# Optimization experiments

Measured on AMD Instinct MI355X. Metric: run time of the kernel, lower is better.

Reference implementation:

```python
import jax, jax.numpy as jnp
import numpy as np

N = 50000  # nodes (spots)


def setup_inputs() -> dict:
    key = jax.random.key(0)
    ks = jax.random.split(key, 10)
    d_gene, d_img, H, Hh, O = 3000, 1024, 512, 256, 64

    def lin(k, i, o):
        return (jax.random.normal(k, (i, o), jnp.float32) / np.sqrt(i).astype(np.float32))

    return {
        "gene_data": jax.random.normal(ks[0], (N, d_gene), jnp.float32),
        "image_data": jax.random.normal(ks[1], (N, d_img), jnp.float32),
        "gene_edge_index": jax.random.randint(ks[2], (2, 800000), 0, N, dtype=jnp.int32).astype(jnp.int64),
        "spatial_edge_index": jax.random.randint(ks[3], (2, 300000), 0, N, dtype=jnp.int32).astype(jnp.int64),
        "W_fc1": lin(ks[4], d_gene, H), "b_fc1": jnp.zeros((H,), jnp.float32),
        "W_fc2": lin(ks[5], d_img, H), "b_fc2": jnp.zeros((H,), jnp.float32),
        "W_g11": lin(ks[6], H, Hh), "b_g11": jnp.zeros((Hh,), jnp.float32),
        "W_g12": lin(ks[7], H, Hh), "b_g12": jnp.zeros((Hh,), jnp.float32),
        "W_g21": lin(ks[8], Hh, O), "b_g21": jnp.zeros((O,), jnp.float32),
        "W_g22": lin(ks[9], Hh, O), "b_g22": jnp.zeros((O,), jnp.float32),
        "w1": jnp.float32(0.5), "w2": jnp.float32(0.5),
    }


def _gcn(x, edge_index, W, b, n):
    # PyG GCNConv: h = x @ W; add self-loops; symmetric norm D^-1/2 (A+I) D^-1/2; scatter-add; + bias
    h = x @ W  # [n, out]
    loop = jnp.arange(n, dtype=edge_index.dtype)
    src = jnp.concatenate([edge_index[0], loop])
    dst = jnp.concatenate([edge_index[1], loop])
    deg = jax.ops.segment_sum(jnp.ones_like(src, x.dtype), dst, num_segments=n)
    dinv = jax.lax.rsqrt(jnp.maximum(deg, jnp.asarray(1e-12, x.dtype)))
    norm = dinv[src] * dinv[dst]  # [E+n]
    out = jax.ops.segment_sum(h[src] * norm[:, None], dst, num_segments=n)
    return out + b


def reference(gene_data, image_data, gene_edge_index, spatial_edge_index,
              W_fc1, b_fc1, W_fc2, b_fc2,
              W_g11, b_g11, W_g12, b_g12,
              W_g21, b_g21, W_g22, b_g22,
              w1, w2):
    n = gene_data.shape[0]
    x1 = jax.nn.relu(gene_data @ W_fc1 + b_fc1)
    x2 = jax.nn.relu(image_data @ W_fc2 + b_fc2)
    # dropout: eval mode -> identity
    h1 = jax.nn.relu(_gcn(x1, spatial_edge_index, W_g11, b_g11, n))
    h2 = jax.nn.relu(_gcn(x2, gene_edge_index, W_g12, b_g12, n))
    x = w1 * h1 + (1.0 - w1) * h2
    o1 = _gcn(x, spatial_edge_index, W_g21, b_g21, n)
    o2 = _gcn(x, gene_edge_index, W_g22, b_g22, n)
    return w2 * o1 + (1.0 - w2) * o2
```

## Files before the change

### kernel.cpp

```cpp
#include <hip/hip_runtime.h>
#include <hip/hip_bf16.h>
#include <stdint.h>

typedef __attribute__((ext_vector_type(4))) float f32x4;
typedef __attribute__((ext_vector_type(8))) short short8;
typedef __attribute__((ext_vector_type(4))) short short4v;

#define CDIV(a, b) (((a) + (b) - 1) / (b))

__device__ __forceinline__ unsigned short f2bf(float x) {
  union { float f; unsigned int u; } c; c.f = x;
  unsigned int r = c.u + 0x7FFFu + ((c.u >> 16) & 1u);
  return (unsigned short)(r >> 16);
}
__device__ __forceinline__ unsigned short f2bf_hw(float x) {
  __hip_bfloat16 h = __float2bfloat16(x);
  unsigned short u; __builtin_memcpy(&u, &h, 2); return u;
}
__device__ __forceinline__ float bf2f(unsigned short b) {
  union { unsigned int u; float f; } c; c.u = (unsigned int)b << 16; return c.f;
}

__device__ __forceinline__ void gl2lds16(const void* g, void* lds) {
  __builtin_amdgcn_global_load_lds(
      reinterpret_cast<const __attribute__((address_space(1))) unsigned int*>(
          reinterpret_cast<uintptr_t>(g)),
      reinterpret_cast<__attribute__((address_space(3))) unsigned int*>(
          reinterpret_cast<uintptr_t>(lds)),
      16, 0, 0);
}

__global__ void transpose_w(const float* __restrict__ W, unsigned short* __restrict__ Wt,
                            int K, int N, int Kpad) {
  __shared__ float tile[32][33];
  int kb = blockIdx.x * 32, nb = blockIdx.y * 32;
  int tx = threadIdx.x & 31, ty = threadIdx.x >> 5;
  for (int r = ty; r < 32; r += 8) {
    int k = kb + r, n = nb + tx;
    tile[r][tx] = (k < K && n < N) ? W[(size_t)k * N + n] : 0.f;
  }
  __syncthreads();
  for (int r = ty; r < 32; r += 8) {
    int n = nb + r, k = kb + tx;
    if (n < N && k < Kpad) Wt[(size_t)n * Kpad + k] = f2bf(tile[tx][r]);
  }
}

__global__ void prep_init(int* __restrict__ dA, int* __restrict__ dB,
                          int* __restrict__ cA, int* __restrict__ cB, int n) {
  int i = blockIdx.x * blockDim.x + threadIdx.x;
  if (i < n) { dA[i] = 1; dB[i] = 1; cA[i] = 0; cB[i] = 0; }
}

__global__ void deg_hist_both(const int* __restrict__ eiA, int EA, int* __restrict__ degA,
                              const int* __restrict__ eiB, int EB, int* __restrict__ degB, int n) {
  int e = blockIdx.x * blockDim.x + threadIdx.x;
  if (e < EA) {
    unsigned int d = (unsigned int)eiA[(size_t)EA + e];
    if (d < (unsigned int)n) atomicAdd(&degA[d], 1);
  } else if (e < EA + EB) {
    int e2 = e - EA;
    unsigned int d = (unsigned int)eiB[(size_t)EB + e2];
    if (d < (unsigned int)n) atomicAdd(&degB[d], 1);
  }
}

__global__ void dinv_both(const int* __restrict__ dA, float* __restrict__ vA,
                          const int* __restrict__ dB, float* __restrict__ vB, int n) {
  int i = blockIdx.x * blockDim.x + threadIdx.x;
  if (i < n) { vA[i] = rsqrtf((float)dA[i]); vB[i] = rsqrtf((float)dB[i]); }
}

__global__ void scan_rowptr_dual(const int* __restrict__ degA, int* __restrict__ rpA,
                                 const int* __restrict__ degB, int* __restrict__ rpB, int n) {
  const int* deg = (blockIdx.x == 0) ? degA : degB;
  int* rp = (blockIdx.x == 0) ? rpA : rpB;
  __shared__ int wsum[16];
  __shared__ int carry_s;
  const int tid = threadIdx.x, lane = tid & 63, w = tid >> 6;
  if (tid == 0) carry_s = 0;
  __syncthreads();
  for (int base = 0; base < n; base += 1024) {
    int i = base + tid;
    int d = (i < n) ? (deg[i] - 1) : 0;
    int v = d;
    #pragma unroll
    for (int off = 1; off < 64; off <<= 1) {
      int t = __shfl_up(v, off, 64);
      if (lane >= off) v += t;
    }
    if (lane == 63) wsum[w] = v;
    __syncthreads();
    int carry = carry_s;
    if (w == 0) {
      int s = (lane < 16) ? wsum[lane] : 0;
      #pragma unroll
      for (int off = 1; off < 16; off <<= 1) {
        int t = __shfl_up(s, off, 64);
        if (lane >= off) s += t;
      }
      if (lane < 16) wsum[lane] = s;
    }
    __syncthreads();
    int woff = (w > 0) ? wsum[w - 1] : 0;
    if (i < n) rp[i] = carry + woff + v - d;
    if (tid == 0) carry_s = carry + wsum[15];
    __syncthreads();
  }
  if (threadIdx.x == 0) rp[n] = carry_s;
}

__global__ void csr_fill_both(const int* __restrict__ eiA, int EA, const int* __restrict__ rpA,
                              int* __restrict__ curA, const float* __restrict__ dvA,
                              int* __restrict__ csA, float* __restrict__ cnA,
                              const int* __restrict__ eiB, int EB, const int* __restrict__ rpB,
                              int* __restrict__ curB, const float* __restrict__ dvB,
                              int* __restrict__ csB, float* __restrict__ cnB, int n) {
  int e = blockIdx.x * blockDim.x + threadIdx.x;
  if (e < EA) {
    unsigned int s = (unsigned int)eiA[e];
    unsigned int d = (unsigned int)eiA[(size_t)EA + e];
    if (s < (unsigned int)n && d < (unsigned int)n) {
      int pos = rpA[d] + atomicAdd(&curA[d], 1);
      csA[pos] = (int)s;
      cnA[pos] = dvA[s] * dvA[d];
    }
  } else if (e < EA + EB) {
    int e2 = e - EA;
    unsigned int s = (unsigned int)eiB[e2];
    unsigned int d = (unsigned int)eiB[(size_t)EB + e2];
    if (s < (unsigned int)n && d < (unsigned int)n) {
      int pos = rpB[d] + atomicAdd(&curB[d], 1);
      csB[pos] = (int)s;
      cnB[pos] = dvB[s] * dvB[d];
    }
  }
}

template<int BM, int BN, int TH, int NT_N, int AMODE, bool ADD_BIAS, bool DO_RELU>
__global__ __launch_bounds__(TH, 2)
void gemm7(const void* __restrict__ Av, const unsigned short* __restrict__ Bt,
           const float* __restrict__ bias, unsigned short* __restrict__ C,
           int NT_M, int M, int N, int K, int Kpad) {
  constexpr int BK = 64;
  constexpr int WN = TH / 64;
  constexpr int WCOLS = BN / WN;
  constexpr int FM = BM / 16, FN = WCOLS / 16;
  constexpr int BIT  = (BN * 8) / TH;
  constexpr int AIT1 = (BM * 8) / TH;
  constexpr int AIT3 = (BM * 16) / TH;
  constexpr int LOGN = (NT_N == 4) ? 2 : (NT_N == 2 ? 1 : 0);

  const int bid = blockIdx.x;
  const int xcd = bid & 7, j = bid >> 3;
  const int per = (NT_M + 7) >> 3;
  const int mt = xcd * per + (j >> LOGN);
  const int nt = j & (NT_N - 1);
  if (mt >= NT_M) return;
  const int gm = mt * BM, gn = nt * BN;

  constexpr int ABYTES = (AMODE == 3) ? BM * BK * 4 : BM * BK * 2;
  __shared__ __align__(16) char AldsRaw[ABYTES];
  __shared__ __align__(16) unsigned short Blds[BN * BK];

  const int tid = threadIdx.x;
  const int wid = tid >> 6, lane = tid & 63;
  const int kg = lane >> 4, lr = lane & 15;
  const int sx = lr & 7;

  f32x4 acc[FM][FN] = {};

  const int nkt = Kpad / BK;
  for (int kt = 0; kt < nkt; ++kt) {
    const int k0 = kt * BK;
    if constexpr (AMODE == 1) {
      const unsigned short* A = (const unsigned short*)Av;
      unsigned short* Alds = (unsigned short*)AldsRaw;
      #pragma unroll
      for (int it = 0; it < AIT1; ++it) {
        int q = it * TH + tid;
        int r = q >> 3, s = q & 7;
        int grow = gm + r; if (grow > M - 1) grow = M - 1;
        gl2lds16(A + (size_t)grow * K + k0 + ((s ^ (r & 7)) << 3), &Alds[q * 8]);
      }
    } else {
      const float* A = (const float*)Av;
      float* Af = (float*)AldsRaw;
      if (k0 + BK <= K) {
        #pragma unroll
        for (int it = 0; it < AIT3; ++it) {
          int q = it * TH + tid;
          int r = q >> 4, s = q & 15;
          int grow = gm + r; if (grow > M - 1) grow = M - 1;
          gl2lds16(A + (size_t)grow * K + k0 + ((s ^ (r & 15)) << 2), &Af[q * 4]);
        }
      } else {
        #pragma unroll
        for (int it = 0; it < AIT3; ++it) {
          int q = it * TH + tid;
          int r = q >> 4, s = q & 15;
          int grow = gm + r; if (grow > M - 1) grow = M - 1;
          int kbase = k0 + ((s ^ (r & 15)) << 2);
          f32x4 v = {0.f, 0.f, 0.f, 0.f};
          if (kbase + 4 <= K) v = *(const f32x4*)(A + (size_t)grow * K + kbase);
          *(f32x4*)(&Af[q * 4]) = v;
        }
      }
    }
    #pragma unroll
    for (int it = 0; it < BIT; ++it) {
      int q = it * TH + tid;
      int r = q >> 3, s = q & 7;
      gl2lds16(Bt + (size_t)(gn + r) * Kpad + k0 + ((s ^ (r & 7)) << 3), &Blds[q * 8]);
    }
    __syncthreads();
    #pragma unroll
    for (int ks = 0; ks < 2; ++ks) {
      const int k8 = ks * 4 + kg;
      short8 af[FM];
      #pragma unroll
      for (int m = 0; m < FM; m++) {
        int r = m * 16 + lr;
        if constexpr (AMODE == 1) {
          const unsigned short* Alds = (const unsigned short*)AldsRaw;
          af[m] = *(const short8*)(&Alds[(r * 8 + (k8 ^ sx)) * 8]);
        } else {
          const float* Af = (const float*)AldsRaw;
          int s0 = (2 * k8) ^ lr, s1 = (2 * k8 + 1) ^ lr;
          f32x4 lo = *(const f32x4*)(Af + r * 64 + s0 * 4);
          f32x4 hi = *(const f32x4*)(Af + r * 64 + s1 * 4);
          #pragma unroll
          for (int i = 0; i < 4; i++) {
            af[m][i]     = (short)f2bf_hw(lo[i]);
            af[m][i + 4] = (short)f2bf_hw(hi[i]);
          }
        }
      }
      #pragma unroll
      for (int n2 = 0; n2 < FN; n2++) {
        int cc = wid * WCOLS + n2 * 16 + lr;
        short8 bq = *(const short8*)(&Blds[(cc * 8 + (k8 ^ sx)) * 8]);
        #pragma unroll
        for (int m = 0; m < FM; m++)
          acc[m][n2] = __builtin_amdgcn_mfma_f32_16x16x32_bf16(af[m], bq, acc[m][n2], 0, 0, 0);
      }
    }
    __syncthreads();
  }
  #pragma unroll
  for (int m = 0; m < FM; m++) {
    #pragma unroll
    for (int jj = 0; jj < 4; jj++) {
      int grow = gm + m * 16 + kg * 4 + jj;
      if (grow < M) {
        #pragma unroll
        for (int n2 = 0; n2 < FN; n2++) {
          int gcol = gn + wid * WCOLS + n2 * 16 + lr;
          float v = acc[m][n2][jj];
          if constexpr (ADD_BIAS) v += bias[gcol];
          if constexpr (DO_RELU) v = fmaxf(v, 0.f);
          C[(size_t)grow * N + gcol] = f2bf(v);
        }
      }
    }
  }
}

template<int F, int LDHA, int LDHB, bool DO_RELU, bool OUT_BF16>
__global__ __launch_bounds__(256)
void scatter_fused(const unsigned short* __restrict__ hA, const unsigned short* __restrict__ hB,
                   const int* __restrict__ rpA, const int* __restrict__ csA,
                   const float* __restrict__ cnA, const float* __restrict__ dvA,
                   const float* __restrict__ bA,
                   const int* __restrict__ rpB, const int* __restrict__ csB,
                   const float* __restrict__ cnB, const float* __restrict__ dvB,
                   const float* __restrict__ bB,
                   const float* __restrict__ wptr, void* __restrict__ outp, int n) {
  constexpr int TPN = F / 4;
  const int tid = threadIdx.x;
  const int node = blockIdx.x * (256 / TPN) + tid / TPN;
  const int c4 = (tid % TPN) * 4;
  if (node >= n) return;

  f32x4 accA, accB, t2 = {0.f, 0.f, 0.f, 0.f};
  {
    float d = dvA[node]; float sc = d * d;
    short4v v = *(const short4v*)(hA + (size_t)node * LDHA + c4);
    accA[0] = sc * bf2f((unsigned short)v[0]);
    accA[1] = sc * bf2f((unsigned short)v[1]);
    accA[2] = sc * bf2f((unsigned short)v[2]);
    accA[3] = sc * bf2f((unsigned short)v[3]);
    const int e1 = rpA[node + 1];
    int e = rpA[node];
    for (; e + 2 <= e1; e += 2) {
      int s0 = csA[e], s1 = csA[e + 1];
      float n0 = cnA[e], n1 = cnA[e + 1];
      short4v v0 = *(const short4v*)(hA + (size_t)s0 * LDHA + c4);
      short4v v1 = *(const short4v*)(hA + (size_t)s1 * LDHA + c4);
      accA[0] += n0 * bf2f((unsigned short)v0[0]); t2[0] += n1 * bf2f((unsigned short)v1[0]);
      accA[1] += n0 * bf2f((unsigned short)v0[1]); t2[1] += n1 * bf2f((unsigned short)v1[1]);
      accA[2] += n0 * bf2f((unsigned short)v0[2]); t2[2] += n1 * bf2f((unsigned short)v1[2]);
      accA[3] += n0 * bf2f((unsigned short)v0[3]); t2[3] += n1 * bf2f((unsigned short)v1[3]);
    }
    if (e < e1) {
      int s0 = csA[e]; float n0 = cnA[e];
      short4v v0 = *(const short4v*)(hA + (size_t)s0 * LDHA + c4);
      accA[0] += n0 * bf2f((unsigned short)v0[0]);
      accA[1] += n0 * bf2f((unsigned short)v0[1]);
      accA[2] += n0 * bf2f((unsigned short)v0[2]);
      accA[3] += n0 * bf2f((unsigned short)v0[3]);
    }
    #pragma unroll
    for (int i = 0; i < 4; i++) { accA[i] += t2[i]; t2[i] = 0.f; }
  }
  {
    float d = dvB[node]; float sc = d * d;
    short4v v = *(const short4v*)(hB + (size_t)node * LDHB + c4);
    accB[0] = sc * bf2f((unsigned short)v[0]);
    accB[1] = sc * bf2f((unsigned short)v[1]);
    accB[2] = sc * bf2f((unsigned short)v[2]);
    accB[3] = sc * bf2f((unsigned short)v[3]);
    const int e1 = rpB[node + 1];
    int e = rpB[node];
    for (; e + 2 <= e1; e += 2) {
      int s0 = csB[e], s1 = csB[e + 1];
      float n0 = cnB[e], n1 = cnB[e + 1];
      short4v v0 = *(const short4v*)(hB + (size_t)s0 * LDHB + c4);
      short4v v1 = *(const short4v*)(hB + (size_t)s1 * LDHB + c4);
      accB[0] += n0 * bf2f((unsigned short)v0[0]); t2[0] += n1 * bf2f((unsigned short)v1[0]);
      accB[1] += n0 * bf2f((unsigned short)v0[1]); t2[1] += n1 * bf2f((unsigned short)v1[1]);
      accB[2] += n0 * bf2f((unsigned short)v0[2]); t2[2] += n1 * bf2f((unsigned short)v1[2]);
      accB[3] += n0 * bf2f((unsigned short)v0[3]); t2[3] += n1 * bf2f((unsigned short)v1[3]);
    }
    if (e < e1) {
      int s0 = csB[e]; float n0 = cnB[e];
      short4v v0 = *(const short4v*)(hB + (size_t)s0 * LDHB + c4);
      accB[0] += n0 * bf2f((unsigned short)v0[0]);
      accB[1] += n0 * bf2f((unsigned short)v0[1]);
      accB[2] += n0 * bf2f((unsigned short)v0[2]);
      accB[3] += n0 * bf2f((unsigned short)v0[3]);
    }
    #pragma unroll
    for (int i = 0; i < 4; i++) accB[i] += t2[i];
  }
  f32x4 bvA = *(const f32x4*)(bA + c4);
  f32x4 bvB = *(const f32x4*)(bB + c4);
  float w = *wptr;
  size_t idx = (size_t)node * F + c4;
  f32x4 r;
  #pragma unroll
  for (int i = 0; i < 4; i++) {
    float va = accA[i] + bvA[i];
    float vb = accB[i] + bvB[i];
    if constexpr (DO_RELU) { va = fmaxf(va, 0.f); vb = fmaxf(vb, 0.f); }
    r[i] = w * va + (1.f - w) * vb;
  }
  if constexpr (OUT_BF16) {
    short4v o;
    o[0] = (short)f2bf(r[0]); o[1] = (short)f2bf(r[1]);
    o[2] = (short)f2bf(r[2]); o[3] = (short)f2bf(r[3]);
    *(short4v*)((unsigned short*)outp + idx) = o;
  } else {
    *(f32x4*)((float*)outp + idx) = r;
  }
}

extern "C" void kernel_launch(void* const* d_in, const int* in_sizes, int n_in,
                              void* d_out, int out_size, void* d_ws, size_t ws_size,
                              hipStream_t stream) {
  const float* gene  = (const float*)d_in[0];
  const float* img   = (const float*)d_in[1];
  const int* ei_ge = (const int*)d_in[2];
  const int* ei_sp = (const int*)d_in[3];
  const float* W_fc1 = (const float*)d_in[4];  const float* b_fc1 = (const float*)d_in[5];
  const float* W_fc2 = (const float*)d_in[6];  const float* b_fc2 = (const float*)d_in[7];
  const float* W_g11 = (const float*)d_in[8];  const float* b_g11 = (const float*)d_in[9];
  const float* W_g12 = (const float*)d_in[10]; const float* b_g12 = (const float*)d_in[11];
  const float* W_g21 = (const float*)d_in[12]; const float* b_g21 = (const float*)d_in[13];
  const float* W_g22 = (const float*)d_in[14]; const float* b_g22 = (const float*)d_in[15];
  const float* w1p   = (const float*)d_in[16];
  const float* w2p   = (const float*)d_in[17];

  const int Nn = 50000;
  const int E_ge = in_sizes[2] / 2;
  const int E_sp = in_sizes[3] / 2;
  const int NT_M = CDIV(Nn, 64);
  const int PER  = CDIV(NT_M, 8);
  const int G1   = 8 * PER;
  const int G2   = 8 * PER * 2;

  char* ws = (char*)d_ws;
  size_t off = 0;
  auto alloc = [&](size_t bytes) -> void* {
    void* p = ws + off;
    off += (bytes + 255) & ~(size_t)255;
    return p;
  };

  unsigned short* Wt1  = (unsigned short*)alloc((size_t)512 * 3008 * 2);
  unsigned short* Wt2  = (unsigned short*)alloc((size_t)512 * 1024 * 2);
  unsigned short* Wt11 = (unsigned short*)alloc((size_t)256 * 512 * 2);
  unsigned short* Wt12 = (unsigned short*)alloc((size_t)256 * 512 * 2);
  unsigned short* WtC  = (unsigned short*)alloc((size_t)128 * 256 * 2);
  int*   deg_sp  = (int*)alloc((size_t)Nn * 4);
  int*   deg_ge  = (int*)alloc((size_t)Nn * 4);
  float* dinv_sp = (float*)alloc((size_t)Nn * 4);
  float* dinv_ge = (float*)alloc((size_t)Nn * 4);
  int*   rp_sp   = (int*)alloc((size_t)(Nn + 1) * 4);
  int*   rp_ge   = (int*)alloc((size_t)(Nn + 1) * 4);
  int*   cur_sp  = (int*)alloc((size_t)Nn * 4);
  int*   cur_ge  = (int*)alloc((size_t)Nn * 4);
  int*   csrc_sp = (int*)alloc((size_t)E_sp * 4);
  float* cnrm_sp = (float*)alloc((size_t)E_sp * 4);
  int*   csrc_ge = (int*)alloc((size_t)E_ge * 4);
  float* cnrm_ge = (float*)alloc((size_t)E_ge * 4);
  unsigned short* xbuf1 = (unsigned short*)alloc((size_t)Nn * 512 * 2);
  unsigned short* xbuf2 = (unsigned short*)alloc((size_t)Nn * 512 * 2);
  unsigned short* tmpA  = (unsigned short*)alloc((size_t)Nn * 256 * 2);
  unsigned short* tmpB  = (unsigned short*)alloc((size_t)Nn * 256 * 2);
  unsigned short* Xc    = xbuf1;
  unsigned short* tmp2  = tmpA;
  (void)ws_size; (void)n_in; (void)out_size;

  transpose_w<<<dim3(94, 16), 256, 0, stream>>>(W_fc1, Wt1, 3000, 512, 3008);
  transpose_w<<<dim3(32, 16), 256, 0, stream>>>(W_fc2, Wt2, 1024, 512, 1024);
  transpose_w<<<dim3(16, 8),  256, 0, stream>>>(W_g11, Wt11, 512, 256, 512);
  transpose_w<<<dim3(16, 8),  256, 0, stream>>>(W_g12, Wt12, 512, 256, 512);
  transpose_w<<<dim3(8, 2),   256, 0, stream>>>(W_g21, WtC, 256, 64, 256);
  transpose_w<<<dim3(8, 2),   256, 0, stream>>>(W_g22, WtC + (size_t)64 * 256, 256, 64, 256);

  prep_init<<<CDIV(Nn, 256), 256, 0, stream>>>(deg_sp, deg_ge, cur_sp, cur_ge, Nn);
  deg_hist_both<<<CDIV(E_sp + E_ge, 256), 256, 0, stream>>>(
      ei_sp, E_sp, deg_sp, ei_ge, E_ge, deg_ge, Nn);
  dinv_both<<<CDIV(Nn, 256), 256, 0, stream>>>(deg_sp, dinv_sp, deg_ge, dinv_ge, Nn);
  scan_rowptr_dual<<<2, 1024, 0, stream>>>(deg_sp, rp_sp, deg_ge, rp_ge, Nn);
  csr_fill_both<<<CDIV(E_sp + E_ge, 256), 256, 0, stream>>>(
      ei_sp, E_sp, rp_sp, cur_sp, dinv_sp, csrc_sp, cnrm_sp,
      ei_ge, E_ge, rp_ge, cur_ge, dinv_ge, csrc_ge, cnrm_ge, Nn);

  gemm7<64, 256, 256, 2, 3, true, true><<<G2, 256, 0, stream>>>(
      gene, Wt1, b_fc1, xbuf1, NT_M, Nn, 512, 3000, 3008);
  gemm7<64, 256, 256, 2, 3, true, true><<<G2, 256, 0, stream>>>(
      img, Wt2, b_fc2, xbuf2, NT_M, Nn, 512, 1024, 1024);
  gemm7<64, 256, 256, 1, 1, false, false><<<G1, 256, 0, stream>>>(
      xbuf1, Wt11, nullptr, tmpA, NT_M, Nn, 256, 512, 512);
  gemm7<64, 256, 256, 1, 1, false, false><<<G1, 256, 0, stream>>>(
      xbuf2, Wt12, nullptr, tmpB, NT_M, Nn, 256, 512, 512);
  scatter_fused<256, 256, 256, true, true><<<Nn / 4, 256, 0, stream>>>(
      tmpA, tmpB, rp_sp, csrc_sp, cnrm_sp, dinv_sp, b_g11,
      rp_ge, csrc_ge, cnrm_ge, dinv_ge, b_g12, w1p, Xc, Nn);
  gemm7<64, 128, 256, 1, 1, false, false><<<G1, 256, 0, stream>>>(
      Xc, WtC, nullptr, tmp2, NT_M, Nn, 128, 256, 256);
  scatter_fused<64, 128, 128, false, false><<<Nn / 16, 256, 0, stream>>>(
      tmp2, tmp2 + 64, rp_sp, csrc_sp, cnrm_sp, dinv_sp, b_g21,
      rp_ge, csrc_ge, cnrm_ge, dinv_ge, b_g22, w2p, d_out, Nn);
}
```

Baseline: 836.1 us.

## Merge paired GEMMs into single launches and unroll gather loop by four

The two independent first-layer GEMMs (gene and image) and the two second-layer GEMMs each run in one launch, with the block index picking which problem a block handles. This removes launch gaps and lets the shorter problem's blocks fill the GPU alongside the longer one's tail. The neighbour gather in the scatter kernel is moved into a helper that unrolls by four with independent accumulators for more memory-level parallelism, at some cost in register use. A simplified gemm7 without the fp32-A path is kept for the last GEMM.

```diff
diff --git a/kernel.cpp b/kernel.cpp
--- a/kernel.cpp
+++ b/kernel.cpp
@@ -139,9 +139,11 @@
 
 template<int BM, int BN, int TH, int NT_N, int AMODE, bool ADD_BIAS, bool DO_RELU>
 __global__ __launch_bounds__(TH, 2)
-void gemm7(const void* __restrict__ Av, const unsigned short* __restrict__ Bt,
-           const float* __restrict__ bias, unsigned short* __restrict__ C,
-           int NT_M, int M, int N, int K, int Kpad) {
+void gemm_pair(const void* __restrict__ A0, const unsigned short* __restrict__ Bt0,
+               const float* __restrict__ b0, unsigned short* __restrict__ C0, int K0, int Kp0,
+               const void* __restrict__ A1, const unsigned short* __restrict__ Bt1,
+               const float* __restrict__ b1, unsigned short* __restrict__ C1, int K1, int Kp1,
+               int split, int NT_M, int M, int N) {
   constexpr int BK = 64;
   constexpr int WN = TH / 64;
   constexpr int WCOLS = BN / WN;
@@ -151,7 +153,16 @@
   constexpr int AIT3 = (BM * 16) / TH;
   constexpr int LOGN = (NT_N == 4) ? 2 : (NT_N == 2 ? 1 : 0);
 
-  const int bid = blockIdx.x;
+  const int bid0 = blockIdx.x;
+  const bool j1 = (bid0 >= split);
+  const int bid = j1 ? (bid0 - split) : bid0;
+  const void* Av = j1 ? A1 : A0;
+  const unsigned short* Bt = j1 ? Bt1 : Bt0;
+  const float* bias = j1 ? b1 : b0;
+  unsigned short* C = j1 ? C1 : C0;
+  const int K = j1 ? K1 : K0;
+  const int Kpad = j1 ? Kp1 : Kp0;
+
   const int xcd = bid & 7, j = bid >> 3;
   const int per = (NT_M + 7) >> 3;
   const int mt = xcd * per + (j >> LOGN);
@@ -266,6 +277,139 @@
   }
 }
 
+template<int BM, int BN, int TH, int NT_N, int AMODE, bool ADD_BIAS, bool DO_RELU>
+__global__ __launch_bounds__(TH, 2)
+void gemm7(const void* __restrict__ Av, const unsigned short* __restrict__ Bt,
+           const float* __restrict__ bias, unsigned short* __restrict__ C,
+           int NT_M, int M, int N, int K, int Kpad) {
+  constexpr int BK = 64;
+  constexpr int WN = TH / 64;
+  constexpr int WCOLS = BN / WN;
+  constexpr int FM = BM / 16, FN = WCOLS / 16;
+  constexpr int BIT  = (BN * 8) / TH;
+  constexpr int AIT1 = (BM * 8) / TH;
+  constexpr int LOGN = (NT_N == 2) ? 1 : 0;
+
+  const int bid = blockIdx.x;
+  const int xcd = bid & 7, j = bid >> 3;
+  const int per = (NT_M + 7) >> 3;
+  const int mt = xcd * per + (j >> LOGN);
+  const int nt = j & (NT_N - 1);
+  if (mt >= NT_M) return;
+  const int gm = mt * BM, gn = nt * BN;
+
+  __shared__ __align__(16) unsigned short Alds[BM * BK];
+  __shared__ __align__(16) unsigned short Blds[BN * BK];
+
+  const int tid = threadIdx.x;
+  const int wid = tid >> 6, lane = tid & 63;
+  const int kg = lane >> 4, lr = lane & 15;
+  const int sx = lr & 7;
+
+  f32x4 acc[FM][FN] = {};
+
+  const int nkt = Kpad / BK;
+  for (int kt = 0; kt < nkt; ++kt) {
+    const int k0 = kt * BK;
+    const unsigned short* A = (const unsigned short*)Av;
+    #pragma unroll
+    for (int it = 0; it < AIT1; ++it) {
+      int q = it * TH + tid;
+      int r = q >> 3, s = q & 7;
+      int grow = gm + r; if (grow > M - 1) grow = M - 1;
+      gl2lds16(A + (size_t)grow * K + k0 + ((s ^ (r & 7)) << 3), &Alds[q * 8]);
+    }
+    #pragma unroll
+    for (int it = 0; it < BIT; ++it) {
+      int q = it * TH + tid;
+      int r = q >> 3, s = q & 7;
+      gl2lds16(Bt + (size_t)(gn + r) * Kpad + k0 + ((s ^ (r & 7)) << 3), &Blds[q * 8]);
+    }
+    __syncthreads();
+    #pragma unroll
+    for (int ks = 0; ks < 2; ++ks) {
+      const int k8 = ks * 4 + kg;
+      short8 af[FM];
+      #pragma unroll
+      for (int m = 0; m < FM; m++) {
+        int r = m * 16 + lr;
+        af[m] = *(const short8*)(&Alds[(r * 8 + (k8 ^ sx)) * 8]);
+      }
+      #pragma unroll
+      for (int n2 = 0; n2 < FN; n2++) {
+        int cc = wid * WCOLS + n2 * 16 + lr;
+        short8 bq = *(const short8*)(&Blds[(cc * 8 + (k8 ^ sx)) * 8]);
+        #pragma unroll
+        for (int m = 0; m < FM; m++)
+          acc[m][n2] = __builtin_amdgcn_mfma_f32_16x16x32_bf16(af[m], bq, acc[m][n2], 0, 0, 0);
+      }
+    }
+    __syncthreads();
+  }
+  #pragma unroll
+  for (int m = 0; m < FM; m++) {
+    #pragma unroll
+    for (int jj = 0; jj < 4; jj++) {
+      int grow = gm + m * 16 + kg * 4 + jj;
+      if (grow < M) {
+        #pragma unroll
+        for (int n2 = 0; n2 < FN; n2++) {
+          int gcol = gn + wid * WCOLS + n2 * 16 + lr;
+          float v = acc[m][n2][jj];
+          if constexpr (ADD_BIAS) v += bias[gcol];
+          if constexpr (DO_RELU) v = fmaxf(v, 0.f);
+          C[(size_t)grow * N + gcol] = f2bf(v);
+        }
+      }
+    }
+  }
+}
+
+template<int LDH>
+__device__ __forceinline__ f32x4 gcn_gather(const unsigned short* __restrict__ h,
+                                            const int* __restrict__ rp,
+                                            const int* __restrict__ cs,
+                                            const float* __restrict__ cn,
+                                            const float* __restrict__ dv,
+                                            int node, int c4) {
+  float d = dv[node];
+  float sc = d * d;
+  f32x4 a0, a1 = {0.f,0.f,0.f,0.f}, a2 = {0.f,0.f,0.f,0.f}, a3 = {0.f,0.f,0.f,0.f};
+  {
+    short4v v = *(const short4v*)(h + (size_t)node * LDH + c4);
+    a0[0] = sc * bf2f((unsigned short)v[0]);
+    a0[1] = sc * bf2f((unsigned short)v[1]);
+    a0[2] = sc * bf2f((unsigned short)v[2]);
+    a0[3] = sc * bf2f((unsigned short)v[3]);
+  }
+  int e = rp[node];
+  const int e1 = rp[node + 1];
+  for (; e + 4 <= e1; e += 4) {
+    int s0 = cs[e], s1 = cs[e+1], s2 = cs[e+2], s3 = cs[e+3];
+    float n0 = cn[e], n1 = cn[e+1], n2 = cn[e+2], n3 = cn[e+3];
+    short4v v0 = *(const short4v*)(h + (size_t)s0 * LDH + c4);
+    short4v v1 = *(const short4v*)(h + (size_t)s1 * LDH + c4);
+    short4v v2 = *(const short4v*)(h + (size_t)s2 * LDH + c4);
+    short4v v3 = *(const short4v*)(h + (size_t)s3 * LDH + c4);
+    #pragma unroll
+    for (int i = 0; i < 4; i++) {
+      a0[i] += n0 * bf2f((unsigned short)v0[i]);
+      a1[i] += n1 * bf2f((unsigned short)v1[i]);
+      a2[i] += n2 * bf2f((unsigned short)v2[i]);
+      a3[i] += n3 * bf2f((unsigned short)v3[i]);
+    }
+  }
+  for (; e < e1; ++e) {
+    int s0 = cs[e]; float n0 = cn[e];
+    short4v v0 = *(const short4v*)(h + (size_t)s0 * LDH + c4);
+    #pragma unroll
+    for (int i = 0; i < 4; i++) a0[i] += n0 * bf2f((unsigned short)v0[i]);
+  }
+  #pragma unroll
+  for (int i = 0; i < 4; i++) a0[i] += a1[i] + a2[i] + a3[i];
+  return a0;
+}
+
 template<int F, int LDHA, int LDHB, bool DO_RELU, bool OUT_BF16>
 __global__ __launch_bounds__(256)
 void scatter_fused(const unsigned short* __restrict__ hA, const unsigned short* __restrict__ hB,
@@ -282,67 +426,9 @@
   const int c4 = (tid % TPN) * 4;
   if (node >= n) return;
 
-  f32x4 accA, accB, t2 = {0.f, 0.f, 0.f, 0.f};
-  {
-    float d = dvA[node]; float sc = d * d;
-    short4v v = *(const short4v*)(hA + (size_t)node * LDHA + c4);
-    accA[0] = sc * bf2f((unsigned short)v[0]);
-    accA[1] = sc * bf2f((unsigned short)v[1]);
-    accA[2] = sc * bf2f((unsigned short)v[2]);
-    accA[3] = sc * bf2f((unsigned short)v[3]);
-    const int e1 = rpA[node + 1];
-    int e = rpA[node];
-    for (; e + 2 <= e1; e += 2) {
-      int s0 = csA[e], s1 = csA[e + 1];
-      float n0 = cnA[e], n1 = cnA[e + 1];
-      short4v v0 = *(const short4v*)(hA + (size_t)s0 * LDHA + c4);
-      short4v v1 = *(const short4v*)(hA + (size_t)s1 * LDHA + c4);
-      accA[0] += n0 * bf2f((unsigned short)v0[0]); t2[0] += n1 * bf2f((unsigned short)v1[0]);
-      accA[1] += n0 * bf2f((unsigned short)v0[1]); t2[1] += n1 * bf2f((unsigned short)v1[1]);
-      accA[2] += n0 * bf2f((unsigned short)v0[2]); t2[2] += n1 * bf2f((unsigned short)v1[2]);
-      accA[3] += n0 * bf2f((unsigned short)v0[3]); t2[3] += n1 * bf2f((unsigned short)v1[3]);
-    }
-    if (e < e1) {
-      int s0 = csA[e]; float n0 = cnA[e];
-      short4v v0 = *(const short4v*)(hA + (size_t)s0 * LDHA + c4);
-      accA[0] += n0 * bf2f((unsigned short)v0[0]);
-      accA[1] += n0 * bf2f((unsigned short)v0[1]);
-      accA[2] += n0 * bf2f((unsigned short)v0[2]);
-      accA[3] += n0 * bf2f((unsigned short)v0[3]);
-    }
-    #pragma unroll
-    for (int i = 0; i < 4; i++) { accA[i] += t2[i]; t2[i] = 0.f; }
-  }
-  {
-    float d = dvB[node]; float sc = d * d;
-    short4v v = *(const short4v*)(hB + (size_t)node * LDHB + c4);
-    accB[0] = sc * bf2f((unsigned short)v[0]);
-    accB[1] = sc * bf2f((unsigned short)v[1]);
-    accB[2] = sc * bf2f((unsigned short)v[2]);
-    accB[3] = sc * bf2f((unsigned short)v[3]);
-    const int e1 = rpB[node + 1];
-    int e = rpB[node];
-    for (; e + 2 <= e1; e += 2) {
-      int s0 = csB[e], s1 = csB[e + 1];
-      float n0 = cnB[e], n1 = cnB[e + 1];
-      short4v v0 = *(const short4v*)(hB + (size_t)s0 * LDHB + c4);
-      short4v v1 = *(const short4v*)(hB + (size_t)s1 * LDHB + c4);
-      accB[0] += n0 * bf2f((unsigned short)v0[0]); t2[0] += n1 * bf2f((unsigned short)v1[0]);
-      accB[1] += n0 * bf2f((unsigned short)v0[1]); t2[1] += n1 * bf2f((unsigned short)v1[1]);
-      accB[2] += n0 * bf2f((unsigned short)v0[2]); t2[2] += n1 * bf2f((unsigned short)v1[2]);
-      accB[3] += n0 * bf2f((unsigned short)v0[3]); t2[3] += n1 * bf2f((unsigned short)v1[3]);
-    }
-    if (e < e1) {
-      int s0 = csB[e]; float n0 = cnB[e];
-      short4v v0 = *(const short4v*)(hB + (size_t)s0 * LDHB + c4);
-      accB[0] += n0 * bf2f((unsigned short)v0[0]);
-      accB[1] += n0 * bf2f((unsigned short)v0[1]);
-      accB[2] += n0 * bf2f((unsigned short)v0[2]);
-      accB[3] += n0 * bf2f((unsigned short)v0[3]);
-    }
-    #pragma unroll
-    for (int i = 0; i < 4; i++) accB[i] += t2[i];
-  }
+  f32x4 accA = gcn_gather<LDHA>(hA, rpA, csA, cnA, dvA, node, c4);
+  f32x4 accB = gcn_gather<LDHB>(hB, rpB, csB, cnB, dvB, node, c4);
+
   f32x4 bvA = *(const f32x4*)(bA + c4);
   f32x4 bvB = *(const f32x4*)(bB + c4);
   float w = *wptr;
@@ -438,14 +524,14 @@
       ei_sp, E_sp, rp_sp, cur_sp, dinv_sp, csrc_sp, cnrm_sp,
       ei_ge, E_ge, rp_ge, cur_ge, dinv_ge, csrc_ge, cnrm_ge, Nn);
 
-  gemm7<64, 256, 256, 2, 3, true, true><<<G2, 256, 0, stream>>>(
-      gene, Wt1, b_fc1, xbuf1, NT_M, Nn, 512, 3000, 3008);
-  gemm7<64, 256, 256, 2, 3, true, true><<<G2, 256, 0, stream>>>(
-      img, Wt2, b_fc2, xbuf2, NT_M, Nn, 512, 1024, 1024);
-  gemm7<64, 256, 256, 1, 1, false, false><<<G1, 256, 0, stream>>>(
-      xbuf1, Wt11, nullptr, tmpA, NT_M, Nn, 256, 512, 512);
-  gemm7<64, 256, 256, 1, 1, false, false><<<G1, 256, 0, stream>>>(
-      xbuf2, Wt12, nullptr, tmpB, NT_M, Nn, 256, 512, 512);
+  gemm_pair<64, 256, 256, 2, 3, true, true><<<2 * G2, 256, 0, stream>>>(
+      gene, Wt1, b_fc1, xbuf1, 3000, 3008,
+      img,  Wt2, b_fc2, xbuf2, 1024, 1024,
+      G2, NT_M, Nn, 512);
+  gemm_pair<64, 256, 256, 1, 1, false, false><<<2 * G1, 256, 0, stream>>>(
+      xbuf1, Wt11, nullptr, tmpA, 512, 512,
+      xbuf2, Wt12, nullptr, tmpB, 512, 512,
+      G1, NT_M, Nn, 256);
   scatter_fused<256, 256, 256, true, true><<<Nn / 4, 256, 0, stream>>>(
       tmpA, tmpB, rp_sp, csrc_sp, cnrm_sp, dinv_sp, b_g11,
       rp_ge, csrc_ge, cnrm_ge, dinv_ge, b_g12, w1p, Xc, Nn);
```

Measured after the change: 736.7 us (median of 2 runs). 1.13x faster.
